# Kernel optimization log

Measured on AMD Instinct MI355X. Metric: run time of the kernel, lower is better.

## Reference

```python
import jax, jax.numpy as jnp
import numpy as np

HEAD_SIZE = 64


def q_shift_multihead(x, ph, pw, head_dim=HEAD_SIZE, shift=1):
    # x: [B, T, C], T == ph*pw. Quarter-wise spatial shifts per head channel block.
    B, T, C = x.shape
    a = jnp.transpose(x, (0, 2, 1)).reshape(B, C // head_dim, head_dim, ph, pw)
    q = head_dim // 4
    out = jnp.zeros_like(a)
    out = out.at[:, :, 0:q, :, shift:].set(a[:, :, 0:q, :, :-shift])          # shift right in W
    out = out.at[:, :, q:2 * q, :, :-shift].set(a[:, :, q:2 * q, :, shift:])  # shift left in W
    out = out.at[:, :, 2 * q:3 * q, shift:, :].set(a[:, :, 2 * q:3 * q, :-shift, :])  # shift down in H
    out = out.at[:, :, 3 * q:, :-shift, :].set(a[:, :, 3 * q:, shift:, :])            # shift up in H
    return jnp.transpose(out.reshape(B, C, T), (0, 2, 1))


def wkv6(r, k, v, w, u):
    # RWKV-6 linear recurrence. r,k,v,w: [B,T,C]; u: [H, hs]. Decay applied as exp(-exp(w)).
    B, T, C = r.shape
    H, hs = C // HEAD_SIZE, HEAD_SIZE
    rh = jnp.transpose(r.reshape(B, T, H, hs), (1, 0, 2, 3))
    kh = jnp.transpose(k.reshape(B, T, H, hs), (1, 0, 2, 3))
    vh = jnp.transpose(v.reshape(B, T, H, hs), (1, 0, 2, 3))
    wh = jnp.exp(-jnp.exp(jnp.transpose(w.reshape(B, T, H, hs), (1, 0, 2, 3))))

    def step(S, inp):  # S: [B,H,hs(key j),hs(val i)]
        rt, kt, vt, wt = inp
        kv = kt[..., :, None] * vt[..., None, :]                # [B,H,hs,hs]
        y = jnp.einsum('bhj,bhji->bhi', rt, S + u[None, :, :, None] * kv)
        return wt[..., None] * S + kv, y

    S0 = jnp.zeros((B, H, hs, hs), r.dtype)
    _, ys = jax.lax.scan(step, S0, (rh, kh, vh, wh))
    return jnp.transpose(ys, (1, 0, 2, 3)).reshape(B, T, C)


def group_norm(x, weight, bias, n_groups, eps=1e-5):
    # x: [N, C]
    N, C = x.shape
    g = x.reshape(N, n_groups, C // n_groups)
    mu = g.mean(-1, keepdims=True)
    var = ((g - mu) ** 2).mean(-1, keepdims=True)
    g = (g - mu) / jnp.sqrt(var + eps)
    return g.reshape(N, C) * weight + bias


def setup_inputs() -> dict:
    key = jax.random.key(0)
    B, ph, pw, C = 8, 32, 32, 768
    T = ph * pw
    n_layer, layer_id = 12, 6
    H = C // HEAD_SIZE
    ks = jax.random.split(key, 10)
    x = jax.random.normal(ks[0], (B, T, C), jnp.float32)
    W_r = 0.02 * jax.random.normal(ks[1], (C, C), jnp.float32)
    W_k = 0.02 * jax.random.normal(ks[2], (C, C), jnp.float32)
    W_v = 0.02 * jax.random.normal(ks[3], (C, C), jnp.float32)
    W_g = 0.02 * jax.random.normal(ks[4], (C, C), jnp.float32)
    W_o = 0.02 * jax.random.normal(ks[5], (C, C), jnp.float32)
    r01 = layer_id / (n_layer - 1)
    r10 = 1.0 - layer_id / n_layer
    ddd = np.arange(C, dtype=np.float64) / C
    maa_x = jnp.asarray(1.0 - ddd ** r10, jnp.float32).reshape(1, 1, C)
    maa_w = maa_x
    maa_k = maa_x
    maa_v = jnp.asarray(1.0 - (ddd ** r10 + 0.3 * r01), jnp.float32).reshape(1, 1, C)
    maa_r = jnp.asarray(1.0 - ddd ** (0.5 * r10), jnp.float32).reshape(1, 1, C)
    maa_g = maa_r
    maa_w1 = jax.random.uniform(ks[6], (C, 32 * 5), jnp.float32, -1e-4, 1e-4)
    maa_w2 = jax.random.uniform(ks[7], (5, 32, C), jnp.float32, -1e-4, 1e-4)
    n = np.arange(C, dtype=np.float64)
    time_decay = jnp.asarray(-6 + 5 * (n / (C - 1)) ** (0.7 + 1.3 * r01), jnp.float32).reshape(1, 1, C)
    dec_w1 = jax.random.uniform(ks[8], (C, 64), jnp.float32, -1e-4, 1e-4)
    dec_w2 = jax.random.uniform(ks[9], (64, C), jnp.float32, -1e-4, 1e-4)
    zig = ((n + 1) % 3 - 1) * 0.1
    faaaa = jnp.asarray(r01 * (1 - n / (C - 1)) + zig, jnp.float32).reshape(H, HEAD_SIZE)
    ln_w = jnp.ones((C,), jnp.float32)
    ln_b = jnp.zeros((C,), jnp.float32)
    return dict(x=x, W_r=W_r, W_k=W_k, W_v=W_v, W_g=W_g, W_o=W_o,
                maa_x=maa_x, maa_w=maa_w, maa_k=maa_k, maa_v=maa_v, maa_r=maa_r, maa_g=maa_g,
                maa_w1=maa_w1, maa_w2=maa_w2, time_decay=time_decay,
                dec_w1=dec_w1, dec_w2=dec_w2, faaaa=faaaa, ln_w=ln_w, ln_b=ln_b,
                patch_h=ph, patch_w=pw)


def reference(x, W_r, W_k, W_v, W_g, W_o, maa_x, maa_w, maa_k, maa_v, maa_r, maa_g,
              maa_w1, maa_w2, time_decay, dec_w1, dec_w2, faaaa, ln_w, ln_b,
              patch_h, patch_w):
    B, T, C = x.shape
    xx = q_shift_multihead(x, patch_h, patch_w) - x
    xxx = x + xx * maa_x
    t = jnp.tanh(xxx @ maa_w1).reshape(B, T, 5, 32)
    m = jnp.einsum('btfr,frc->fbtc', t, maa_w2)  # [5,B,T,C]
    mw, mk, mv, mr, mg = m[0], m[1], m[2], m[3], m[4]
    xw = x + xx * (maa_w + mw)
    xk = x + xx * (maa_k + mk)
    xv = x + xx * (maa_v + mv)
    xr = x + xx * (maa_r + mr)
    xg = x + xx * (maa_g + mg)
    r = xr @ W_r.T
    k = xk @ W_k.T
    v = xv @ W_v.T
    g = jax.nn.relu(xg @ W_g.T)
    ww = jnp.tanh(xw @ dec_w1) @ dec_w2
    w = time_decay + ww
    y = wkv6(r, k, v, w, faaaa)
    y = group_norm(y.reshape(B * T, C), ln_w, ln_b, C // HEAD_SIZE).reshape(B, T, C)
    return (y * g) @ W_o.T
```

## Files before the change

### kernel.cpp

```cpp
#include <hip/hip_runtime.h>
#include <math.h>


#define EPI_NONE 0
#define EPI_TANH 1
#define EPI_RELU 2
#define EPI_BIAS 3

typedef float f32x4 __attribute__((ext_vector_type(4)));
typedef __bf16 bf16x8 __attribute__((ext_vector_type(8)));

__device__ __forceinline__ ushort f2bf(float x) {
  unsigned u = __float_as_uint(x);
  return (ushort)((u + 0x7fffu + ((u >> 16) & 1u)) >> 16);
}

#define GLDS16(gp, lp)                                                   \
  __builtin_amdgcn_global_load_lds(                                      \
      (const __attribute__((address_space(1))) void*)(gp),               \
      (__attribute__((address_space(3))) void*)(lp), 16, 0, 0)

__global__ __launch_bounds__(256) void k_prep(
    const float* __restrict__ x, const float* __restrict__ maa_x,
    ushort* __restrict__ xxx_bf,
    const float* __restrict__ w1, const float* __restrict__ w2,
    const float* __restrict__ dw1, const float* __restrict__ dw2,
    ushort* __restrict__ maa1T, ushort* __restrict__ w2T,
    ushort* __restrict__ w1dT, ushort* __restrict__ w2dT,
    int B, int T, int C, int ph, int pw) {
  long bx = blockIdx.x;
  const long QBLK = 24576;
  if (bx < QBLK) {
    long idx = bx * 256 + threadIdx.x;
    int c = (int)(idx % C);
    long bt = idx / C;
    int t = (int)(bt % T);
    int quarter = (c & 63) >> 4;
    int hh = t / pw;
    int ww = t - hh * pw;
    long rowbase = (bt - t) * C;
    float sval = 0.f;
    int st = -1;
    if (quarter == 0)      { if (ww >= 1)      st = t - 1;  }
    else if (quarter == 1) { if (ww < pw - 1)  st = t + 1;  }
    else if (quarter == 2) { if (hh >= 1)      st = t - pw; }
    else                   { if (hh < ph - 1)  st = t + pw; }
    if (st >= 0) sval = x[rowbase + (long)st * C + c];
    float xval = x[idx];
    float d = sval - xval;
    xxx_bf[idx] = f2bf(xval + d * maa_x[c]);
    return;
  }
  int idx = (int)(bx - QBLK) * 256 + threadIdx.x;
  if (idx < 196608) {
    int n = idx / 768, k = idx - n * 768;
    maa1T[idx] = f2bf(n < 160 ? w1[(size_t)k * 160 + n] : 0.f);
  } else if (idx < 196608 + 122880) {
    int j = idx - 196608;
    int c = j / 160, kk = j - c * 160;
    w2T[j] = f2bf(w2[(size_t)kk * 768 + c]);
  } else if (idx < 196608 + 122880 + 98304) {
    int j = idx - (196608 + 122880);
    int n = j / 768, k = j - n * 768;
    w1dT[j] = f2bf(n < 64 ? dw1[(size_t)k * 64 + n] : 0.f);
  } else {
    int j = idx - (196608 + 122880 + 98304);
    int n = j >> 6, k = j & 63;
    w2dT[j] = f2bf(dw2[(size_t)k * 768 + n]);
  }
}

__global__ __launch_bounds__(256) void k_mix5m(
    const ushort* __restrict__ t5b, const ushort* __restrict__ w2T,
    const float* __restrict__ x,
    const float* __restrict__ maa_w, const float* __restrict__ maa_k,
    const float* __restrict__ maa_v, const float* __restrict__ maa_r,
    const float* __restrict__ maa_g,
    ushort* __restrict__ xw, ushort* __restrict__ xk, ushort* __restrict__ xvb,
    ushort* __restrict__ xr, ushort* __restrict__ xg,
    int C, int T, int ph, int pw) {
  int tid = threadIdx.x;
  int lane = tid & 63, wid = tid >> 6;
  int m0 = blockIdx.y * 64, n0 = blockIdx.x * 128;
  int lm = lane & 15, lk = (lane >> 4) * 8;
  int rq = (lane >> 4) * 4;
  const ushort* ap = t5b + (size_t)(m0 + wid * 16 + lm) * 160 + lk;

  int stq[4][4];
#pragma unroll
  for (int q = 0; q < 4; q++) {
    int mr = m0 + wid * 16 + rq + q;
    int t = mr % T;
    int hh = t / pw, ww = t - hh * pw;
    stq[q][0] = (ww >= 1)      ? mr - 1  : -1;
    stq[q][1] = (ww < pw - 1)  ? mr + 1  : -1;
    stq[q][2] = (hh >= 1)      ? mr - pw : -1;
    stq[q][3] = (hh < ph - 1)  ? mr + pw : -1;
  }

  float xh[8][4], dh[8][4];
#pragma unroll
  for (int j = 0; j < 8; j++)
#pragma unroll
    for (int q = 0; q < 4; q++) {
      int mr = m0 + wid * 16 + rq + q;
      int col = n0 + j * 16 + lm;
      float xv = x[(size_t)mr * C + col];
      int sr = stq[q][j & 3];
      float sv = (sr >= 0) ? x[(size_t)sr * C + col] : 0.f;
      xh[j][q] = xv;
      dh[j][q] = sv - xv;
    }

#pragma unroll
  for (int f = 0; f < 5; f++) {
    bf16x8 af = *(const bf16x8*)(ap + f * 32);
    f32x4 acc[8];
#pragma unroll
    for (int j = 0; j < 8; j++) {
      bf16x8 bfj = *(const bf16x8*)(w2T +
          (size_t)(n0 + j * 16 + lm) * 160 + f * 32 + lk);
      acc[j] = __builtin_amdgcn_mfma_f32_16x16x32_bf16(
          af, bfj, (f32x4){0.f, 0.f, 0.f, 0.f}, 0, 0, 0);
    }
    const float* maa_f = (f == 0) ? maa_w : (f == 1) ? maa_k
                        : (f == 2) ? maa_v : (f == 3) ? maa_r : maa_g;
    ushort* dst = (f == 0) ? xw : (f == 1) ? xk
                 : (f == 2) ? xvb : (f == 3) ? xr : xg;
#pragma unroll
    for (int j = 0; j < 8; j++) {
      float mf = maa_f[n0 + j * 16 + lm];
#pragma unroll
      for (int q = 0; q < 4; q++) {
        size_t off = (size_t)(m0 + wid * 16 + rq + q) * C + (n0 + j * 16 + lm);
        dst[off] = f2bf(xh[j][q] + dh[j][q] * (mf + acc[j][q]));
      }
    }
  }
}

__global__ __launch_bounds__(256) void k_cvt5(
    const float* __restrict__ s0, const float* __restrict__ s1,
    const float* __restrict__ s2, const float* __restrict__ s3,
    const float* __restrict__ s4,
    ushort* __restrict__ d0, ushort* __restrict__ d1,
    ushort* __restrict__ d2, ushort* __restrict__ d3,
    ushort* __restrict__ d4, int n) {
  const float* s;
  ushort* d;
  switch (blockIdx.y) {
    case 0: s = s0; d = d0; break;
    case 1: s = s1; d = d1; break;
    case 2: s = s2; d = d2; break;
    case 3: s = s3; d = d3; break;
    default: s = s4; d = d4; break;
  }
  int i = (blockIdx.x * 256 + threadIdx.x) * 4;
  if (i >= n) return;
  float4 v = *(const float4*)(s + i);
  ushort4 o;
  o.x = f2bf(v.x); o.y = f2bf(v.y); o.z = f2bf(v.z); o.w = f2bf(v.w);
  *(ushort4*)(d + i) = o;
}

template <int EPI, bool NMASK, bool OBF16>
__global__ __launch_bounds__(256) void k_gemm_bf(
    const ushort* __restrict__ A, const ushort* __restrict__ W,
    const float* __restrict__ bias, void* __restrict__ Cm,
    int M, int N, int K) {
  __shared__ ushort Al[128 * 64];
  __shared__ ushort Bl[128 * 64];
  int nwg = gridDim.x * gridDim.y;
  int bid = blockIdx.y * gridDim.x + blockIdx.x;
  int swz = (nwg & 7) == 0 ? ((bid & 7) * (nwg >> 3) + (bid >> 3)) : bid;
  int bx = swz % gridDim.x, by = swz / gridDim.x;
  int m0 = by * 128, n0 = bx * 128;
  int tid = threadIdx.x;
  int lane = tid & 63, wave = tid >> 6;
  int wm = (wave >> 1) * 64, wn = (wave & 1) * 64;
  int lm = lane & 15, g = lane >> 4;
  f32x4 acc[4][4];
#pragma unroll
  for (int i = 0; i < 4; i++)
#pragma unroll
    for (int j = 0; j < 4; j++) acc[i][j] = (f32x4){0.f, 0.f, 0.f, 0.f};

  for (int k0 = 0; k0 < K; k0 += 64) {
#pragma unroll
    for (int i = 0; i < 4; i++) {
      int cid = tid + i * 256;
      int row = cid >> 3, p = cid & 7;
      int cq = p ^ (row & 7);
      GLDS16(A + (size_t)(m0 + row) * K + k0 + cq * 8, Al + cid * 8);
      GLDS16(W + (size_t)(n0 + row) * K + k0 + cq * 8, Bl + cid * 8);
    }
    __syncthreads();
#pragma unroll
    for (int s = 0; s < 2; s++) {
      bf16x8 af[4], bf[4];
#pragma unroll
      for (int i = 0; i < 4; i++) {
        int r = wm + i * 16 + lm;
        af[i] = *(const bf16x8*)&Al[r * 64 + (((s * 4 + g) ^ (r & 7)) * 8)];
        int rb = wn + i * 16 + lm;
        bf[i] = *(const bf16x8*)&Bl[rb * 64 + (((s * 4 + g) ^ (rb & 7)) * 8)];
      }
#pragma unroll
      for (int i = 0; i < 4; i++)
#pragma unroll
        for (int j = 0; j < 4; j++)
          acc[i][j] = __builtin_amdgcn_mfma_f32_16x16x32_bf16(
              af[i], bf[j], acc[i][j], 0, 0, 0);
    }
    __syncthreads();
  }
  int rq = (lane >> 4) * 4;
#pragma unroll
  for (int i = 0; i < 4; i++) {
#pragma unroll
    for (int j = 0; j < 4; j++) {
      int gn = n0 + wn + j * 16 + lm;
      if (NMASK && gn >= N) continue;
      float bv = (EPI == EPI_BIAS) ? bias[gn] : 0.f;
#pragma unroll
      for (int q = 0; q < 4; q++) {
        int gm = m0 + wm + i * 16 + rq + q;
        float val = acc[i][j][q];
        if (EPI == EPI_BIAS) val += bv;
        if (EPI == EPI_RELU) val = fmaxf(val, 0.f);
        if (EPI == EPI_TANH) val = tanhf(val);
        if (OBF16) ((ushort*)Cm)[(size_t)gm * N + gn] = f2bf(val);
        else       ((float*)Cm)[(size_t)gm * N + gn] = val;
      }
    }
  }
}

__global__ __launch_bounds__(256) void k_proj4(
    const ushort* __restrict__ A0, const ushort* __restrict__ A1,
    const ushort* __restrict__ A2, const ushort* __restrict__ A3,
    const ushort* __restrict__ W0, const ushort* __restrict__ W1,
    const ushort* __restrict__ W2, const ushort* __restrict__ W3,
    float* __restrict__ C0, float* __restrict__ C1,
    float* __restrict__ C2, float* __restrict__ C3,
    int M, int N, int K) {
  int nwg = gridDim.x;
  int bid = blockIdx.x;
  int swz = (bid & 7) * (nwg >> 3) + (bid >> 3);
  int nxt = N / 128;
  int per_z = (M / 128) * nxt;
  int z = swz / per_z;
  int rem = swz - z * per_z;
  int my = rem / nxt, nx = rem - my * nxt;
  const ushort* A = (z == 0) ? A0 : (z == 1) ? A1 : (z == 2) ? A2 : A3;
  const ushort* W = (z == 0) ? W0 : (z == 1) ? W1 : (z == 2) ? W2 : W3;
  float* Cm       = (z == 0) ? C0 : (z == 1) ? C1 : (z == 2) ? C2 : C3;
  __shared__ ushort Al[128 * 64];
  __shared__ ushort Bl[128 * 64];
  int tid = threadIdx.x;
  int m0 = my * 128, n0 = nx * 128;
  int lane = tid & 63, wave = tid >> 6;
  int wm = (wave >> 1) * 64, wn = (wave & 1) * 64;
  int lm = lane & 15, g = lane >> 4;
  f32x4 acc[4][4];
#pragma unroll
  for (int i = 0; i < 4; i++)
#pragma unroll
    for (int j = 0; j < 4; j++) acc[i][j] = (f32x4){0.f, 0.f, 0.f, 0.f};

  for (int k0 = 0; k0 < K; k0 += 64) {
#pragma unroll
    for (int i = 0; i < 4; i++) {
      int cid = tid + i * 256;
      int row = cid >> 3, p = cid & 7;
      int cq = p ^ (row & 7);
      GLDS16(A + (size_t)(m0 + row) * K + k0 + cq * 8, Al + cid * 8);
      GLDS16(W + (size_t)(n0 + row) * K + k0 + cq * 8, Bl + cid * 8);
    }
    __syncthreads();
#pragma unroll
    for (int s = 0; s < 2; s++) {
      bf16x8 af[4], bf[4];
#pragma unroll
      for (int i = 0; i < 4; i++) {
        int r = wm + i * 16 + lm;
        af[i] = *(const bf16x8*)&Al[r * 64 + (((s * 4 + g) ^ (r & 7)) * 8)];
        int rb = wn + i * 16 + lm;
        bf[i] = *(const bf16x8*)&Bl[rb * 64 + (((s * 4 + g) ^ (rb & 7)) * 8)];
      }
#pragma unroll
      for (int i = 0; i < 4; i++)
#pragma unroll
        for (int j = 0; j < 4; j++)
          acc[i][j] = __builtin_amdgcn_mfma_f32_16x16x32_bf16(
              af[i], bf[j], acc[i][j], 0, 0, 0);
    }
    __syncthreads();
  }
  bool relu = (z == 3);
  int rq = (lane >> 4) * 4;
#pragma unroll
  for (int i = 0; i < 4; i++) {
#pragma unroll
    for (int j = 0; j < 4; j++) {
      int gn = n0 + wn + j * 16 + lm;
#pragma unroll
      for (int q = 0; q < 4; q++) {
        int gm = m0 + wm + i * 16 + rq + q;
        float val = acc[i][j][q];
        if (relu) val = fmaxf(val, 0.f);
        Cm[(size_t)gm * N + gn] = val;
      }
    }
  }
}

__global__ __launch_bounds__(256) void k_wkv_prekv(
    const float* __restrict__ r, const float* __restrict__ k,
    const float* __restrict__ w, const float* __restrict__ u,
    const float* __restrict__ v,
    float* __restrict__ rt, float* __restrict__ kt,
    float* __restrict__ aL, float* __restrict__ pdiag,
    float* __restrict__ kvb, int B, int T, int C, int H, int L) {
  __shared__ float Ks[64 * 64];
  __shared__ float Vs[64 * 64];
  __shared__ float pls[64 * 68];
  __shared__ float gsum[4 * 64];
  int nch = T / L;
  int blk = blockIdx.x;
  int bh = blk / nch, c = blk - bh * nch;
  int b = bh / H, h = bh - b * H;
  int tid = threadIdx.x;
  int gsel = tid >> 6;
  int j = tid & 63;
  long cbase = ((long)b * T + (long)c * L) * C + h * 64;

#pragma unroll
  for (int i = 0; i < 4; i++) {
    int chunk = gsel * 4 + i;
    int row = chunk * 4 + (j >> 4);
    int cq = j & 15;
    GLDS16(v + cbase + (long)row * C + cq * 4, Vs + chunk * 256);
  }

  int tau0 = gsel * 16;
  float uj = u[h * 64 + j];
  float ev[16];
#pragma unroll
  for (int i = 0; i < 16; i++)
    ev[i] = expf(w[cbase + (long)(tau0 + i) * C + j]);
  float pre[16];
  float run = 0.f;
#pragma unroll
  for (int i = 0; i < 16; i++) { pre[i] = run; run += ev[i]; }
  gsum[gsel * 64 + j] = run;
  __syncthreads();
  float s0g = gsum[0 * 64 + j];
  float s1g = gsum[1 * 64 + j];
  float s2g = gsum[2 * 64 + j];
  float off0 = (gsel > 0 ? s0g : 0.f) + (gsel > 1 ? s1g : 0.f) +
               (gsel > 2 ? s2g : 0.f);
  if (gsel == 3)
    aL[((long)bh * nch + c) * 64 + j] = expf(-(off0 + run));

#pragma unroll
  for (int i = 0; i < 16; i++) {
    long offg = cbase + (long)(tau0 + i) * C + j;
    float rv = r[offg];
    float kv = k[offg];
    float ce = off0 + pre[i];
    float rtv = rv * expf(-ce);
    float ktv = kv * expf(ce + ev[i]);
    rt[offg] = rtv;
    kt[offg] = ktv;
    Ks[(tau0 + i) * 64 + j] = ktv;
    pls[(tau0 + i) * 68 + j] = rv * uj * kv;
  }
  __syncthreads();

  if (tid < 64) {
    float s0 = 0.f, s1 = 0.f, s2 = 0.f, s3 = 0.f;
#pragma unroll
    for (int q = 0; q < 16; q++) {
      float4 p4 = *(const float4*)(pls + tid * 68 + q * 4);
      s0 += p4.x; s1 += p4.y; s2 += p4.z; s3 += p4.w;
    }
    pdiag[(long)bh * T + c * L + tid] = (s0 + s1) + (s2 + s3);
  }

  int lane = tid & 63, jg = tid >> 6;
  float acc[16];
#pragma unroll
  for (int q = 0; q < 16; q++) acc[q] = 0.f;
  for (int s = 0; s < 64; s++) {
    float vi = Vs[s * 64 + lane];
#pragma unroll
    for (int q4 = 0; q4 < 4; q4++) {
      float4 kk = *(const float4*)(Ks + s * 64 + jg * 16 + q4 * 4);
      acc[q4 * 4 + 0] = fmaf(kk.x, vi, acc[q4 * 4 + 0]);
      acc[q4 * 4 + 1] = fmaf(kk.y, vi, acc[q4 * 4 + 1]);
      acc[q4 * 4 + 2] = fmaf(kk.z, vi, acc[q4 * 4 + 2]);
      acc[q4 * 4 + 3] = fmaf(kk.w, vi, acc[q4 * 4 + 3]);
    }
  }
  float* out = kvb + ((long)bh * nch + c) * 4096;
#pragma unroll
  for (int q = 0; q < 16; q++) out[(jg * 16 + q) * 64 + lane] = acc[q];
}

__global__ __launch_bounds__(256) void k_wkv_scan(
    const float* __restrict__ kvb, const float* __restrict__ aL,
    float* __restrict__ Scb, int nch) {
  int bh = blockIdx.x >> 4;
  int e = ((blockIdx.x & 15) << 8) + threadIdx.x;
  float S = 0.f;
  for (int c = 0; c < nch; c++) {
    long cb = ((long)bh * nch + c) * 4096 + e;
    Scb[cb] = S;
    S = aL[((long)bh * nch + c) * 64 + (e >> 6)] * (S + kvb[cb]);
  }
}

__global__ __launch_bounds__(256, 3) void k_wkv_intra(
    const float* __restrict__ rt, const float* __restrict__ kt,
    const float* __restrict__ v, const float* __restrict__ pdiag,
    const float* __restrict__ Scb, const float* __restrict__ g,
    const float* __restrict__ ln_w, const float* __restrict__ ln_b,
    ushort* __restrict__ z, int B, int T, int C, int H, int L) {
  int nch = T / L;
  int blk = blockIdx.x;
  int bh = blk / nch, c = blk - bh * nch;
  int b = bh / H, h = bh - b * H;
  __shared__ float KtT[64 * 68];
  __shared__ float RtT[64 * 68];
  __shared__ float Pt[64 * 68];
  int tid = threadIdx.x;
  int lane = tid & 63, wid = tid >> 6;
  long cbase = ((long)b * T + (long)c * L) * C + h * 64;
  const float* scp = Scb + ((long)bh * nch + c) * 4096;

  {
    int t0 = (tid >> 4) * 4;
    int c0s = (tid & 15) * 4;
    float4 ka[4], ra[4];
#pragma unroll
    for (int i = 0; i < 4; i++) {
      ka[i] = *(const float4*)(kt + cbase + (long)(t0 + i) * C + c0s);
      ra[i] = *(const float4*)(rt + cbase + (long)(t0 + i) * C + c0s);
    }
#pragma unroll
    for (int j = 0; j < 4; j++) {
      float4 ko, ro;
      ko.x = ka[0][j]; ko.y = ka[1][j]; ko.z = ka[2][j]; ko.w = ka[3][j];
      ro.x = ra[0][j]; ro.y = ra[1][j]; ro.z = ra[2][j]; ro.w = ra[3][j];
      *(float4*)(KtT + (c0s + j) * 68 + t0) = ko;
      *(float4*)(RtT + (c0s + j) * 68 + t0) = ro;
    }
  }
  __syncthreads();

  {
    int s0 = (tid >> 4) * 4;
    int tau0 = (tid & 15) * 4;
    float4 pd4 = *(const float4*)(pdiag + (long)bh * T + c * L + tau0);
    float p00 = 0.f, p01 = 0.f, p02 = 0.f, p03 = 0.f;
    float p10 = 0.f, p11 = 0.f, p12 = 0.f, p13 = 0.f;
    float p20 = 0.f, p21 = 0.f, p22 = 0.f, p23 = 0.f;
    float p30 = 0.f, p31 = 0.f, p32 = 0.f, p33 = 0.f;
#pragma unroll 4
    for (int cc = 0; cc < 64; cc++) {
      float4 kq = *(const float4*)(KtT + cc * 68 + s0);
      float4 rq = *(const float4*)(RtT + cc * 68 + tau0);
      p00 = fmaf(kq.x, rq.x, p00); p01 = fmaf(kq.x, rq.y, p01);
      p02 = fmaf(kq.x, rq.z, p02); p03 = fmaf(kq.x, rq.w, p03);
      p10 = fmaf(kq.y, rq.x, p10); p11 = fmaf(kq.y, rq.y, p11);
      p12 = fmaf(kq.y, rq.z, p12); p13 = fmaf(kq.y, rq.w, p13);
      p20 = fmaf(kq.z, rq.x, p20); p21 = fmaf(kq.z, rq.y, p21);
      p22 = fmaf(kq.z, rq.z, p22); p23 = fmaf(kq.z, rq.w, p23);
      p30 = fmaf(kq.w, rq.x, p30); p31 = fmaf(kq.w, rq.y, p31);
      p32 = fmaf(kq.w, rq.z, p32); p33 = fmaf(kq.w, rq.w, p33);
    }
#define PMASK(PI0, PI1, PI2, PI3, I)                                       \
    {                                                                      \
      int s = s0 + (I);                                                    \
      float4 o;                                                            \
      o.x = (s < tau0 + 0) ? PI0 : (s == tau0 + 0 ? pd4.x : 0.f);          \
      o.y = (s < tau0 + 1) ? PI1 : (s == tau0 + 1 ? pd4.y : 0.f);          \
      o.z = (s < tau0 + 2) ? PI2 : (s == tau0 + 2 ? pd4.z : 0.f);          \
      o.w = (s < tau0 + 3) ? PI3 : (s == tau0 + 3 ? pd4.w : 0.f);          \
      *(float4*)(Pt + s * 68 + tau0) = o;                                  \
    }
    PMASK(p00, p01, p02, p03, 0)
    PMASK(p10, p11, p12, p13, 1)
    PMASK(p20, p21, p22, p23, 2)
    PMASK(p30, p31, p32, p33, 3)
#undef PMASK
  }
  __syncthreads();

  int row0 = wid * 16 + ((lane >> 4) << 2);
  int c0v = (lane & 15) * 4;
  float4 acc0 = {0.f, 0.f, 0.f, 0.f};
  float4 acc1 = {0.f, 0.f, 0.f, 0.f};
  float4 acc2 = {0.f, 0.f, 0.f, 0.f};
  float4 acc3 = {0.f, 0.f, 0.f, 0.f};
  const float* vp = v + cbase + c0v;
#define FMA2(A, P, V4, R, S4)                          \
  A.x = fmaf(P, V4.x, fmaf(R, S4.x, A.x));             \
  A.y = fmaf(P, V4.y, fmaf(R, S4.y, A.y));             \
  A.z = fmaf(P, V4.z, fmaf(R, S4.z, A.z));             \
  A.w = fmaf(P, V4.w, fmaf(R, S4.w, A.w));
#pragma unroll 4
  for (int j = 0; j < 64; j++) {
    float4 pp = *(const float4*)(Pt + j * 68 + row0);
    float4 rr = *(const float4*)(RtT + j * 68 + row0);
    float4 vv = *(const float4*)(vp + (long)j * C);
    float4 ssv = *(const float4*)(scp + j * 64 + c0v);
    FMA2(acc0, pp.x, vv, rr.x, ssv);
    FMA2(acc1, pp.y, vv, rr.y, ssv);
    FMA2(acc2, pp.z, vv, rr.z, ssv);
    FMA2(acc3, pp.w, vv, rr.w, ssv);
  }
#undef FMA2

  float4 lw4 = *(const float4*)(ln_w + h * 64 + c0v);
  float4 lb4 = *(const float4*)(ln_b + h * 64 + c0v);
#define GNROW(A, m)                                                        \
  {                                                                        \
    float s1 = (A.x + A.y) + (A.z + A.w);                                  \
    s1 += __shfl_xor(s1, 1, 64);                                           \
    s1 += __shfl_xor(s1, 2, 64);                                           \
    s1 += __shfl_xor(s1, 4, 64);                                           \
    s1 += __shfl_xor(s1, 8, 64);                                           \
    float mu = s1 * (1.f / 64.f);                                          \
    float4 dd;                                                             \
    dd.x = A.x - mu; dd.y = A.y - mu; dd.z = A.z - mu; dd.w = A.w - mu;    \
    float s2 = (dd.x * dd.x + dd.y * dd.y) + (dd.z * dd.z + dd.w * dd.w);  \
    s2 += __shfl_xor(s2, 1, 64);                                           \
    s2 += __shfl_xor(s2, 2, 64);                                           \
    s2 += __shfl_xor(s2, 4, 64);                                           \
    s2 += __shfl_xor(s2, 8, 64);                                           \
    float rstd = rsqrtf(s2 * (1.f / 64.f) + 1e-5f);                        \
    long off = cbase + (long)(row0 + m) * C + c0v;                         \
    float4 g4 = *(const float4*)(g + off);                                 \
    ushort4 ob;                                                            \
    ob.x = f2bf((dd.x * rstd * lw4.x + lb4.x) * g4.x);                     \
    ob.y = f2bf((dd.y * rstd * lw4.y + lb4.y) * g4.y);                     \
    ob.z = f2bf((dd.z * rstd * lw4.z + lb4.z) * g4.z);                     \
    ob.w = f2bf((dd.w * rstd * lw4.w + lb4.w) * g4.w);                     \
    *(ushort4*)(z + off) = ob;                                             \
  }
  GNROW(acc0, 0)
  GNROW(acc1, 1)
  GNROW(acc2, 2)
  GNROW(acc3, 3)
#undef GNROW
}

extern "C" void kernel_launch(void* const* d_in, const int* in_sizes, int n_in,
                              void* d_out, int out_size, void* d_ws, size_t ws_size,
                              hipStream_t stream) {
  const int B = 8, T = 1024, C = 768, H = 12, ph = 32, pw = 32;
  const int M = B * T;
  const int L = 64, NCH = T / L;

  const float* x        = (const float*)d_in[0];
  const float* W_r      = (const float*)d_in[1];
  const float* W_k      = (const float*)d_in[2];
  const float* W_v      = (const float*)d_in[3];
  const float* W_g      = (const float*)d_in[4];
  const float* W_o      = (const float*)d_in[5];
  const float* maa_x    = (const float*)d_in[6];
  const float* maa_w    = (const float*)d_in[7];
  const float* maa_k    = (const float*)d_in[8];
  const float* maa_v    = (const float*)d_in[9];
  const float* maa_r    = (const float*)d_in[10];
  const float* maa_g    = (const float*)d_in[11];
  const float* maa_w1   = (const float*)d_in[12];
  const float* maa_w2   = (const float*)d_in[13];
  const float* time_dec = (const float*)d_in[14];
  const float* dec_w1   = (const float*)d_in[15];
  const float* dec_w2   = (const float*)d_in[16];
  const float* faaaa    = (const float*)d_in[17];
  const float* ln_w     = (const float*)d_in[18];
  const float* ln_b     = (const float*)d_in[19];

  float* ws = (float*)d_ws;
  const size_t S = (size_t)M * C;
  float* F0 = ws + 0 * S;
  float* F1 = ws + 1 * S;
  float* F2 = ws + 2 * S;
  float* F3 = ws + 3 * S;
  float* F4 = ws + 4 * S;
  float* F5 = ws + 5 * S;
  float* F6 = ws + 6 * S;
  float* t5    = ws + 7 * S;
  float* t6    = t5 + (size_t)M * 160;
  float* aLb   = t6 + (size_t)M * 64;
  float* pdiag = aLb + (size_t)B * H * NCH * 64;
  float* dec_t = pdiag + (size_t)B * H * T;

  ushort* xxx_bf = (ushort*)F1;
  ushort* xw_bf = (ushort*)F2;
  ushort* xr_bf = (ushort*)F5;
  ushort* xk_bf = xr_bf + S;
  ushort* xv_bf = (ushort*)F6;
  ushort* xg_bf = xv_bf + S;
  float*  kvb   = F6;
  ushort* z_bf  = (ushort*)F6;
  ushort* t5b   = (ushort*)t5;
  ushort* t_bf  = (ushort*)dec_t;
  ushort* w2T   = t_bf + (size_t)M * 64;
  float* Scb = F1;
  const int WSZ = C * C;
  ushort* wr_bf = (ushort*)t5;
  ushort* wk_bf = wr_bf + WSZ;
  ushort* wv_bf = wk_bf + WSZ;
  ushort* wg_bf = wv_bf + WSZ;
  ushort* wo_bf = (ushort*)t6;
  ushort* maa1T = wo_bf + WSZ;
  ushort* w1dT  = maa1T + 256 * 768;
  ushort* w2dT  = w1dT + 128 * 768;

  {
    k_prep<<<24576 + 1824, 256, 0, stream>>>(
        x, maa_x, xxx_bf, maa_w1, maa_w2, dec_w1, dec_w2,
        maa1T, w2T, w1dT, w2dT, B, T, C, ph, pw);
  }
  {
    dim3 grid(2, M / 128);
    k_gemm_bf<EPI_TANH, true, true><<<grid, 256, 0, stream>>>(
        xxx_bf, maa1T, nullptr, t5b, M, 160, C);
  }
  {
    dim3 grid(C / 128, M / 64);
    k_mix5m<<<grid, 256, 0, stream>>>(t5b, w2T, x, maa_w, maa_k, maa_v,
                                      maa_r, maa_g, xw_bf, xk_bf, xv_bf, xr_bf,
                                      xg_bf, C, T, ph, pw);
  }
  {
    dim3 grid((WSZ / 4 + 255) / 256, 5);
    k_cvt5<<<grid, 256, 0, stream>>>(W_r, W_k, W_v, W_g, W_o,
                                     wr_bf, wk_bf, wv_bf, wg_bf, wo_bf, WSZ);
  }
  {
    k_proj4<<<(C / 128) * (M / 128) * 4, 256, 0, stream>>>(
        xr_bf, xk_bf, xv_bf, xg_bf, wr_bf, wk_bf, wv_bf, wg_bf,
        F0, F1, F3, F4, M, C, C);
  }
  {
    dim3 g1(1, M / 128);
    k_gemm_bf<EPI_TANH, true, true><<<g1, 256, 0, stream>>>(
        xw_bf, w1dT, nullptr, t_bf, M, 64, C);
    dim3 g2(C / 128, M / 128);
    k_gemm_bf<EPI_BIAS, false, false><<<g2, 256, 0, stream>>>(
        t_bf, w2dT, time_dec, F2, M, C, 64);
  }
  k_wkv_prekv<<<B * H * NCH, 256, 0, stream>>>(
      F0, F1, F2, faaaa, F3, F5, F2, aLb, pdiag, kvb, B, T, C, H, L);
  k_wkv_scan<<<B * H * 16, 256, 0, stream>>>(kvb, aLb, Scb, NCH);
  k_wkv_intra<<<B * H * NCH, 256, 0, stream>>>(
      F5, F2, F3, pdiag, Scb, F4, ln_w, ln_b, z_bf, B, T, C, H, L);
  {
    dim3 grid(C / 128, M / 128);
    k_gemm_bf<EPI_NONE, false, false><<<grid, 256, 0, stream>>>(
        z_bf, wo_bf, nullptr, (float*)d_out, M, C, C);
  }
}
```

Before: 383.2 us.

## Fuse decay-LoRA first GEMM into proj4 and recompute rt/kt inside intra kernel

```diff
diff --git a/kernel.cpp b/kernel.cpp
--- a/kernel.cpp
+++ b/kernel.cpp
@@ -239,22 +239,31 @@
 __global__ __launch_bounds__(256) void k_proj4(
     const ushort* __restrict__ A0, const ushort* __restrict__ A1,
     const ushort* __restrict__ A2, const ushort* __restrict__ A3,
+    const ushort* __restrict__ A4,
     const ushort* __restrict__ W0, const ushort* __restrict__ W1,
     const ushort* __restrict__ W2, const ushort* __restrict__ W3,
+    const ushort* __restrict__ W4,
     float* __restrict__ C0, float* __restrict__ C1,
     float* __restrict__ C2, float* __restrict__ C3,
+    ushort* __restrict__ C4,
     int M, int N, int K) {
   int nwg = gridDim.x;
   int bid = blockIdx.x;
   int swz = (bid & 7) * (nwg >> 3) + (bid >> 3);
   int nxt = N / 128;
   int per_z = (M / 128) * nxt;
-  int z = swz / per_z;
-  int rem = swz - z * per_z;
-  int my = rem / nxt, nx = rem - my * nxt;
-  const ushort* A = (z == 0) ? A0 : (z == 1) ? A1 : (z == 2) ? A2 : A3;
-  const ushort* W = (z == 0) ? W0 : (z == 1) ? W1 : (z == 2) ? W2 : W3;
-  float* Cm       = (z == 0) ? C0 : (z == 1) ? C1 : (z == 2) ? C2 : C3;
+  int z, my, nx;
+  if (swz < 4 * per_z) {
+    z = swz / per_z;
+    int rem = swz - z * per_z;
+    my = rem / nxt; nx = rem - my * nxt;
+  } else {
+    z = 4; my = swz - 4 * per_z; nx = 0;
+  }
+  const ushort* A = (z == 0) ? A0 : (z == 1) ? A1 : (z == 2) ? A2
+                  : (z == 3) ? A3 : A4;
+  const ushort* W = (z == 0) ? W0 : (z == 1) ? W1 : (z == 2) ? W2
+                  : (z == 3) ? W3 : W4;
   __shared__ ushort Al[128 * 64];
   __shared__ ushort Bl[128 * 64];
   int tid = threadIdx.x;
@@ -297,8 +306,24 @@
     }
     __syncthreads();
   }
+  int rq = (lane >> 4) * 4;
+  if (z == 4) {
+#pragma unroll
+    for (int i = 0; i < 4; i++)
+#pragma unroll
+      for (int j = 0; j < 4; j++) {
+        int gn = wn + j * 16 + lm;
+        if (gn >= 64) continue;
+#pragma unroll
+        for (int q = 0; q < 4; q++) {
+          int gm = m0 + wm + i * 16 + rq + q;
+          C4[(size_t)gm * 64 + gn] = f2bf(tanhf(acc[i][j][q]));
+        }
+      }
+    return;
+  }
+  float* Cm = (z == 0) ? C0 : (z == 1) ? C1 : (z == 2) ? C2 : C3;
   bool relu = (z == 3);
-  int rq = (lane >> 4) * 4;
 #pragma unroll
   for (int i = 0; i < 4; i++) {
 #pragma unroll
@@ -316,15 +341,12 @@
 }
 
 __global__ __launch_bounds__(256) void k_wkv_prekv(
-    const float* __restrict__ r, const float* __restrict__ k,
-    const float* __restrict__ w, const float* __restrict__ u,
+    const float* __restrict__ k, const float* __restrict__ w,
     const float* __restrict__ v,
-    float* __restrict__ rt, float* __restrict__ kt,
-    float* __restrict__ aL, float* __restrict__ pdiag,
-    float* __restrict__ kvb, int B, int T, int C, int H, int L) {
+    float* __restrict__ aL, float* __restrict__ kvb,
+    int B, int T, int C, int H, int L) {
   __shared__ float Ks[64 * 64];
   __shared__ float Vs[64 * 64];
-  __shared__ float pls[64 * 68];
   __shared__ float gsum[4 * 64];
   int nch = T / L;
   int blk = blockIdx.x;
@@ -344,7 +366,6 @@
   }
 
   int tau0 = gsel * 16;
-  float uj = u[h * 64 + j];
   float ev[16];
 #pragma unroll
   for (int i = 0; i < 16; i++)
@@ -355,38 +376,18 @@
   for (int i = 0; i < 16; i++) { pre[i] = run; run += ev[i]; }
   gsum[gsel * 64 + j] = run;
   __syncthreads();
-  float s0g = gsum[0 * 64 + j];
-  float s1g = gsum[1 * 64 + j];
-  float s2g = gsum[2 * 64 + j];
-  float off0 = (gsel > 0 ? s0g : 0.f) + (gsel > 1 ? s1g : 0.f) +
-               (gsel > 2 ? s2g : 0.f);
+  float off0 = (gsel > 0 ? gsum[j] : 0.f) +
+               (gsel > 1 ? gsum[64 + j] : 0.f) +
+               (gsel > 2 ? gsum[128 + j] : 0.f);
   if (gsel == 3)
     aL[((long)bh * nch + c) * 64 + j] = expf(-(off0 + run));
 
 #pragma unroll
   for (int i = 0; i < 16; i++) {
-    long offg = cbase + (long)(tau0 + i) * C + j;
-    float rv = r[offg];
-    float kv = k[offg];
-    float ce = off0 + pre[i];
-    float rtv = rv * expf(-ce);
-    float ktv = kv * expf(ce + ev[i]);
-    rt[offg] = rtv;
-    kt[offg] = ktv;
-    Ks[(tau0 + i) * 64 + j] = ktv;
-    pls[(tau0 + i) * 68 + j] = rv * uj * kv;
+    float kv = k[cbase + (long)(tau0 + i) * C + j];
+    Ks[(tau0 + i) * 64 + j] = kv * expf(off0 + pre[i] + ev[i]);
   }
   __syncthreads();
-
-  if (tid < 64) {
-    float s0 = 0.f, s1 = 0.f, s2 = 0.f, s3 = 0.f;
-#pragma unroll
-    for (int q = 0; q < 16; q++) {
-      float4 p4 = *(const float4*)(pls + tid * 68 + q * 4);
-      s0 += p4.x; s1 += p4.y; s2 += p4.z; s3 += p4.w;
-    }
-    pdiag[(long)bh * T + c * L + tid] = (s0 + s1) + (s2 + s3);
-  }
 
   int lane = tid & 63, jg = tid >> 6;
   float acc[16];
@@ -422,9 +423,10 @@
 }
 
 __global__ __launch_bounds__(256, 3) void k_wkv_intra(
-    const float* __restrict__ rt, const float* __restrict__ kt,
-    const float* __restrict__ v, const float* __restrict__ pdiag,
-    const float* __restrict__ Scb, const float* __restrict__ g,
+    const float* __restrict__ r, const float* __restrict__ k,
+    const float* __restrict__ w, const float* __restrict__ u,
+    const float* __restrict__ v, const float* __restrict__ Scb,
+    const float* __restrict__ g,
     const float* __restrict__ ln_w, const float* __restrict__ ln_b,
     ushort* __restrict__ z, int B, int T, int C, int H, int L) {
   int nch = T / L;
@@ -434,35 +436,59 @@
   __shared__ float KtT[64 * 68];
   __shared__ float RtT[64 * 68];
   __shared__ float Pt[64 * 68];
+  __shared__ float gsum[4 * 64];
+  __shared__ float pdv[64];
   int tid = threadIdx.x;
   int lane = tid & 63, wid = tid >> 6;
   long cbase = ((long)b * T + (long)c * L) * C + h * 64;
   const float* scp = Scb + ((long)bh * nch + c) * 4096;
 
   {
-    int t0 = (tid >> 4) * 4;
-    int c0s = (tid & 15) * 4;
-    float4 ka[4], ra[4];
-#pragma unroll
-    for (int i = 0; i < 4; i++) {
-      ka[i] = *(const float4*)(kt + cbase + (long)(t0 + i) * C + c0s);
-      ra[i] = *(const float4*)(rt + cbase + (long)(t0 + i) * C + c0s);
-    }
-#pragma unroll
-    for (int j = 0; j < 4; j++) {
-      float4 ko, ro;
-      ko.x = ka[0][j]; ko.y = ka[1][j]; ko.z = ka[2][j]; ko.w = ka[3][j];
-      ro.x = ra[0][j]; ro.y = ra[1][j]; ro.z = ra[2][j]; ro.w = ra[3][j];
-      *(float4*)(KtT + (c0s + j) * 68 + t0) = ko;
-      *(float4*)(RtT + (c0s + j) * 68 + t0) = ro;
-    }
+    int gsel = wid;
+    int j = lane;
+    int tau0p = gsel * 16;
+    float uj = u[h * 64 + j];
+    float ev[16];
+#pragma unroll
+    for (int i = 0; i < 16; i++)
+      ev[i] = expf(w[cbase + (long)(tau0p + i) * C + j]);
+    float pre[16];
+    float run = 0.f;
+#pragma unroll
+    for (int i = 0; i < 16; i++) { pre[i] = run; run += ev[i]; }
+    gsum[gsel * 64 + j] = run;
+    __syncthreads();
+    float off0 = (gsel > 0 ? gsum[j] : 0.f) +
+                 (gsel > 1 ? gsum[64 + j] : 0.f) +
+                 (gsel > 2 ? gsum[128 + j] : 0.f);
+#pragma unroll
+    for (int i = 0; i < 16; i++) {
+      int tau = tau0p + i;
+      long offg = cbase + (long)tau * C + j;
+      float rv = r[offg];
+      float kv = k[offg];
+      float ce = off0 + pre[i];
+      RtT[j * 68 + tau] = rv * expf(-ce);
+      KtT[j * 68 + tau] = kv * expf(ce + ev[i]);
+      Pt[tau * 68 + j] = rv * uj * kv;
+    }
+  }
+  __syncthreads();
+  if (tid < 64) {
+    float s0 = 0.f, s1 = 0.f, s2 = 0.f, s3 = 0.f;
+#pragma unroll
+    for (int q = 0; q < 16; q++) {
+      float4 p4 = *(const float4*)(Pt + tid * 68 + q * 4);
+      s0 += p4.x; s1 += p4.y; s2 += p4.z; s3 += p4.w;
+    }
+    pdv[tid] = (s0 + s1) + (s2 + s3);
   }
   __syncthreads();
 
   {
     int s0 = (tid >> 4) * 4;
     int tau0 = (tid & 15) * 4;
-    float4 pd4 = *(const float4*)(pdiag + (long)bh * T + c * L + tau0);
+    float4 pd4 = *(const float4*)(pdv + tau0);
     float p00 = 0.f, p01 = 0.f, p02 = 0.f, p03 = 0.f;
     float p10 = 0.f, p11 = 0.f, p12 = 0.f, p13 = 0.f;
     float p20 = 0.f, p21 = 0.f, p22 = 0.f, p23 = 0.f;
@@ -608,10 +634,10 @@
   ushort* xg_bf = xv_bf + S;
   float*  kvb   = F6;
   ushort* z_bf  = (ushort*)F6;
+  float*  Scb   = F5;
   ushort* t5b   = (ushort*)t5;
   ushort* t_bf  = (ushort*)dec_t;
   ushort* w2T   = t_bf + (size_t)M * 64;
-  float* Scb = F1;
   const int WSZ = C * C;
   ushort* wr_bf = (ushort*)t5;
   ushort* wk_bf = wr_bf + WSZ;
@@ -644,23 +670,21 @@
                                      wr_bf, wk_bf, wv_bf, wg_bf, wo_bf, WSZ);
   }
   {
-    k_proj4<<<(C / 128) * (M / 128) * 4, 256, 0, stream>>>(
-        xr_bf, xk_bf, xv_bf, xg_bf, wr_bf, wk_bf, wv_bf, wg_bf,
-        F0, F1, F3, F4, M, C, C);
-  }
-  {
-    dim3 g1(1, M / 128);
-    k_gemm_bf<EPI_TANH, true, true><<<g1, 256, 0, stream>>>(
-        xw_bf, w1dT, nullptr, t_bf, M, 64, C);
+    k_proj4<<<(C / 128) * (M / 128) * 4 + (M / 128), 256, 0, stream>>>(
+        xr_bf, xk_bf, xv_bf, xg_bf, xw_bf,
+        wr_bf, wk_bf, wv_bf, wg_bf, w1dT,
+        F0, F1, F3, F4, t_bf, M, C, C);
+  }
+  {
     dim3 g2(C / 128, M / 128);
     k_gemm_bf<EPI_BIAS, false, false><<<g2, 256, 0, stream>>>(
         t_bf, w2dT, time_dec, F2, M, C, 64);
   }
   k_wkv_prekv<<<B * H * NCH, 256, 0, stream>>>(
-      F0, F1, F2, faaaa, F3, F5, F2, aLb, pdiag, kvb, B, T, C, H, L);
+      F1, F2, F3, aLb, kvb, B, T, C, H, L);
   k_wkv_scan<<<B * H * 16, 256, 0, stream>>>(kvb, aLb, Scb, NCH);
   k_wkv_intra<<<B * H * NCH, 256, 0, stream>>>(
-      F5, F2, F3, pdiag, Scb, F4, ln_w, ln_b, z_bf, B, T, C, H, L);
+      F0, F1, F2, faaaa, F3, Scb, F4, ln_w, ln_b, z_bf, B, T, C, H, L);
   {
     dim3 grid(C / 128, M / 128);
     k_gemm_bf<EPI_NONE, false, false><<<grid, 256, 0, stream>>>(
```

Result: faster. 356.9 us (-6.9%).
